# Kernel optimization log

Hardware: AMD Instinct MI355X
Metric: run time of the kernel (lower is better)

The kernel has to match this reference:

```python
import jax, jax.numpy as jnp
import numpy as np

N, E, IN, HID, HEADS, OUT = 50000, 800000, 184, 64, 4, 2
LRELU_SLOPE = 0.2
LN_EPS = 1e-5


def setup_inputs() -> dict:
    key = jax.random.key(0)
    ks = jax.random.split(key, 20)
    p = lambda k, s: jax.random.normal(k, s, jnp.float32) * 0.05
    return {
        'x': jax.random.normal(ks[0], (N, IN), jnp.float32),
        'edge_index': jax.random.randint(ks[1], (2, E), 0, N, jnp.int64),
        'Wp': p(ks[2], (IN, HID)), 'bp': p(ks[3], (HID,)),
        'W0': p(ks[4], (HID, HEADS * HID)), 'as0': p(ks[5], (HEADS, HID)), 'ad0': p(ks[6], (HEADS, HID)), 'b0': p(ks[7], (HEADS * HID,)),
        'W1': p(ks[8], (HEADS * HID, HEADS * HID)), 'as1': p(ks[9], (HEADS, HID)), 'ad1': p(ks[10], (HEADS, HID)), 'b1': p(ks[11], (HEADS * HID,)),
        'W2': p(ks[12], (HEADS * HID, OUT)), 'as2': p(ks[13], (1, OUT)), 'ad2': p(ks[14], (1, OUT)), 'b2': p(ks[15], (OUT,)),
        'ln_g': jnp.ones((HEADS * HID,), jnp.float32), 'ln_b': jnp.zeros((HEADS * HID,), jnp.float32),
    }


def _layernorm(x, g, b):
    mu = jnp.mean(x, axis=-1, keepdims=True)
    var = jnp.mean(jnp.square(x - mu), axis=-1, keepdims=True)
    return (x - mu) * jax.lax.rsqrt(var + LN_EPS) * g + b


def _gat_conv(x, src, dst, n, W, a_s, a_d, b, heads, c):
    # x: [n, in]; PyG GATConv: per-head linear, edge attention, segment softmax over dst, scatter-add
    h = (x @ W).reshape(n, heads, c)                 # [n, H, C]
    al_s = jnp.sum(h * a_s, axis=-1)                  # [n, H]
    al_d = jnp.sum(h * a_d, axis=-1)                  # [n, H]
    e = jax.nn.leaky_relu(al_s[src] + al_d[dst], LRELU_SLOPE)   # [E, H]
    m = jax.ops.segment_max(e, dst, num_segments=n)   # per-dst max (self-loops ensure nonempty)
    ex = jnp.exp(e - m[dst])
    den = jax.ops.segment_sum(ex, dst, num_segments=n)
    alpha = ex / (den[dst] + 1e-16)                   # PyG softmax eps
    msg = h[src] * alpha[:, :, None]                  # [E, H, C]
    out = jax.ops.segment_sum(msg, dst, num_segments=n)
    return out.reshape(n, heads * c) + b


def reference(x, edge_index, Wp, bp, W0, as0, ad0, b0, W1, as1, ad1, b1, W2, as2, ad2, b2, ln_g, ln_b):
    n = x.shape[0]
    loop = jnp.arange(n, dtype=edge_index.dtype)      # add_self_loops=True
    src = jnp.concatenate([edge_index[0], loop])
    dst = jnp.concatenate([edge_index[1], loop])

    h = x @ Wp + bp                                   # input_proj -> [n, HID]
    # layer 0: out dim HID*HEADS==256 -> norm; residual skipped (x_res is [n, HID])
    h = _gat_conv(h, src, dst, n, W0, as0, ad0, b0, HEADS, HID)
    h = jax.nn.elu(_layernorm(h, ln_g, ln_b))
    # dropout: eval mode (identity)
    # layer 1: norm + residual + elu
    h_res = h
    h = _gat_conv(h, src, dst, n, W1, as1, ad1, b1, HEADS, HID)
    h = jax.nn.elu(_layernorm(h, ln_g, ln_b) + h_res)
    # layer 2 (last): heads=1, no norm/activation
    return _gat_conv(h, src, dst, n, W2, as2, ad2, b2, 1, OUT)
```

## Files before the change

### kernel.cpp

```cpp
#include <hip/hip_runtime.h>
#include <hip/hip_bf16.h>
#include <cmath>
#include <cfloat>

constexpr int IN_DIM = 184;
constexpr int KP     = 192;
constexpr int HID    = 64;
constexpr int HEADS  = 4;
constexpr int F1     = HEADS * HID;
constexpr float SLOPE = 0.2f;
constexpr float LN_EPS = 1e-5f;

using short8 = __attribute__((ext_vector_type(8))) short;
using f32x4  = __attribute__((ext_vector_type(4))) float;

__device__ inline float b2f(ushort u) {
    return __uint_as_float(((unsigned)u) << 16);
}
__device__ inline ushort f2b(float f) {
    __hip_bfloat16 b = __float2bfloat16(f);
    return *reinterpret_cast<ushort*>(&b);
}
__device__ inline float lrelu(float e) { return e > 0.f ? e : SLOPE * e; }
__device__ inline float fexp(float x) { return __expf(x); }
__device__ inline float frcp(float x) { return __builtin_amdgcn_rcpf(x); }

__device__ inline size_t frag_idx(int k, int c) {
    int kt = k >> 5, kk = k & 31;
    int q = (kk & 15) >> 2, j = (kk & 3) | ((kk >> 4) << 2);
    int w = c >> 6, ct = (c >> 4) & 3, lr = c & 15;
    int lane = (q << 4) | lr;
    return ((((size_t)kt * 4 + w) * 4 + ct) * 64 + lane) * 8 + j;
}

__device__ inline void edge_sd(const int* __restrict__ ei, int E, int idx, int& s, int& d) {
    if (idx < E) { s = ei[idx]; d = ei[E + idx]; }
    else         { s = idx - E; d = idx - E; }
}

__global__ __launch_bounds__(256) void weight_prep(const float* __restrict__ Wp,
                                                   const float* __restrict__ W0,
                                                   const float* __restrict__ bp,
                                                   const float* __restrict__ W1,
                                                   ushort* __restrict__ Wf0,
                                                   float* __restrict__ bc,
                                                   ushort* __restrict__ Wf1,
                                                   const int* __restrict__ ei,
                                                   int E, int Etot,
                                                   int* __restrict__ deg) {
    int b = blockIdx.x, c = threadIdx.x;
    if (b < KP) {
        int k = b;
        float s = 0.f;
        if (k < IN_DIM)
            for (int j = 0; j < HID; ++j) s = fmaf(Wp[k * HID + j], W0[j * F1 + c], s);
        Wf0[frag_idx(k, c)] = f2b(s);
        if (k == 0) {
            float bs = 0.f;
            for (int j = 0; j < HID; ++j) bs = fmaf(bp[j], W0[j * F1 + c], bs);
            bc[c] = bs;
        }
    } else if (b < KP + F1) {
        int k = b - KP;
        Wf1[frag_idx(k, c)] = f2b(W1[(size_t)k * F1 + c]);
    } else {
        int idx = (b - KP - F1) * 256 + c;
        if (idx < Etot) {
            int s, d; edge_sd(ei, E, idx, s, d);
            atomicAdd(&deg[d], 1);
        }
    }
}

template<int KSTEPS, bool L0>
__global__ __launch_bounds__(256) void mfma_gemm2(const void* __restrict__ Xv,
                                                  const ushort* __restrict__ Wfrag,
                                                  const float* __restrict__ bc,
                                                  const float* __restrict__ as_,
                                                  const float* __restrict__ ad_,
                                                  unsigned char* __restrict__ F8,
                                                  float* __restrict__ rscale,
                                                  float* __restrict__ als,
                                                  float* __restrict__ ald,
                                                  int M,
                                                  int gemm_blocks,
                                                  const int* __restrict__ ei,
                                                  int E, int Etot,
                                                  int* __restrict__ wcur,
                                                  int* __restrict__ csr_src) {
    const int tid = threadIdx.x;
    int tile;

    if constexpr (L0) {
        const int bid = blockIdx.x;
        const int gq = bid / 3, gr = bid - gq * 3;
        const bool is_gemm = (gr == 0) && (gq < gemm_blocks);
        if (!is_gemm) {
            int fid = bid - min(gq + (gr ? 1 : 0) + (gr == 0 ? 1 : 0) - (gr == 0 ? 1 : 0), 0);
            int ng = min(gq + (gr > 0 ? 1 : 0), gemm_blocks);
            if (gr == 0 && gq >= gemm_blocks) ng = gemm_blocks;
            fid = bid - ng - (gr == 0 && gq < gemm_blocks ? 1 : 0);
            int base = fid * 512 + tid;
#pragma unroll
            for (int r = 0; r < 2; ++r) {
                int idx = base + r * 256;
                if (idx < Etot) {
                    int s, d; edge_sd(ei, E, idx, s, d);
                    int pos = atomicAdd(&wcur[d], 1);
                    csr_src[pos] = s;
                }
            }
            return;
        }
        tile = gq;
    } else {
        tile = blockIdx.x;
    }

    const int w = tid >> 6, l = tid & 63;
    const int lr = l & 15, q = l >> 4;
    const int row0 = tile * 64;

    __shared__ ushort a_lds[2][64][40];
    __shared__ float rmax_lds[64][4];

    const int srow = tid >> 2, seg = tid & 3;
    int grow = row0 + srow; if (grow >= M) grow = M - 1;

    auto stage = [&](int buf, int kt) {
        if constexpr (!L0) {
            const ushort* p = (const ushort*)Xv + (size_t)grow * 256 + kt * 32 + seg * 8;
            *(uint4*)&a_lds[buf][srow][seg * 8] = *(const uint4*)p;
        } else {
            int kb = kt * 32 + seg * 8;
            uint4 o = {0u, 0u, 0u, 0u};
            if (kb < IN_DIM) {
                const float* p = (const float*)Xv + (size_t)grow * IN_DIM + kb;
                float4 lo = *(const float4*)p;
                float4 hi = *(const float4*)(p + 4);
                o.x = (uint)f2b(lo.x) | ((uint)f2b(lo.y) << 16);
                o.y = (uint)f2b(lo.z) | ((uint)f2b(lo.w) << 16);
                o.z = (uint)f2b(hi.x) | ((uint)f2b(hi.y) << 16);
                o.w = (uint)f2b(hi.z) | ((uint)f2b(hi.w) << 16);
            }
            *(uint4*)&a_lds[buf][srow][seg * 8] = o;
        }
    };

    f32x4 acc[4][4] = {};

    stage(0, 0);
    short8 bcur[4];
#pragma unroll
    for (int ct = 0; ct < 4; ++ct) {
        const ushort* bp = Wfrag + ((((size_t)0 * 4 + w) * 4 + ct) * 64 + l) * 8;
        short8 b; *(uint4*)&b = *(const uint4*)bp; bcur[ct] = b;
    }
    __syncthreads();

    int buf = 0;
#pragma unroll
    for (int kt = 0; kt < KSTEPS; ++kt) {
        short8 bnext[4];
        if (kt + 1 < KSTEPS) {
#pragma unroll
            for (int ct = 0; ct < 4; ++ct) {
                const ushort* bp = Wfrag + ((((size_t)(kt + 1) * 4 + w) * 4 + ct) * 64 + l) * 8;
                short8 b; *(uint4*)&b = *(const uint4*)bp; bnext[ct] = b;
            }
            stage(buf ^ 1, kt + 1);
        }
        short8 afr[4];
#pragma unroll
        for (int rt = 0; rt < 4; ++rt) {
            short8 a;
            *(uint2*)&a       = *(const uint2*)&a_lds[buf][rt * 16 + lr][4 * q];
            *((uint2*)&a + 1) = *(const uint2*)&a_lds[buf][rt * 16 + lr][4 * q + 16];
            afr[rt] = a;
        }
#pragma unroll
        for (int rt = 0; rt < 4; ++rt)
#pragma unroll
            for (int ct = 0; ct < 4; ++ct)
                acc[rt][ct] = __builtin_amdgcn_mfma_f32_16x16x32_bf16(afr[rt], bcur[ct], acc[rt][ct], 0, 0, 0);
        __syncthreads();
        if (kt + 1 < KSTEPS) {
#pragma unroll
            for (int ct = 0; ct < 4; ++ct) bcur[ct] = bnext[ct];
        }
        buf ^= 1;
    }

    if constexpr (L0) {
        float bcv[4];
#pragma unroll
        for (int ct = 0; ct < 4; ++ct) bcv[ct] = bc[w * 64 + ct * 16 + lr];
#pragma unroll
        for (int rt = 0; rt < 4; ++rt)
#pragma unroll
            for (int ct = 0; ct < 4; ++ct)
#pragma unroll
                for (int r = 0; r < 4; ++r) acc[rt][ct][r] += bcv[ct];
    }

#pragma unroll
    for (int rt = 0; rt < 4; ++rt) {
#pragma unroll
        for (int r = 0; r < 4; ++r) {
            float m = fmaxf(fmaxf(fabsf(acc[rt][0][r]), fabsf(acc[rt][1][r])),
                            fmaxf(fabsf(acc[rt][2][r]), fabsf(acc[rt][3][r])));
            m = fmaxf(m, __shfl_xor(m, 1));
            m = fmaxf(m, __shfl_xor(m, 2));
            m = fmaxf(m, __shfl_xor(m, 4));
            m = fmaxf(m, __shfl_xor(m, 8));
            if (lr == 0) rmax_lds[rt * 16 + q * 4 + r][w] = m;
        }
    }
    __syncthreads();

#pragma unroll
    for (int rt = 0; rt < 4; ++rt) {
#pragma unroll
        for (int r = 0; r < 4; ++r) {
            int lrow = rt * 16 + q * 4 + r;
            float m = fmaxf(fmaxf(rmax_lds[lrow][0], rmax_lds[lrow][1]),
                            fmaxf(rmax_lds[lrow][2], rmax_lds[lrow][3]));
            float inv = (m > 0.f) ? 127.f / m : 0.f;
            int row = row0 + lrow;
            if (row < M) {
#pragma unroll
                for (int ct = 0; ct < 4; ++ct) {
                    int qv = (int)rintf(acc[rt][ct][r] * inv) + 128;
                    qv = min(max(qv, 0), 255);
                    F8[(size_t)row * 256 + w * 64 + ct * 16 + lr] = (unsigned char)qv;
                }
                if (w == 0 && lr == 0) rscale[row] = m * (1.f / 127.f);
            }
        }
    }

    float asv[4], adv[4];
#pragma unroll
    for (int ct = 0; ct < 4; ++ct) {
        asv[ct] = as_[w * 64 + ct * 16 + lr];
        adv[ct] = ad_[w * 64 + ct * 16 + lr];
    }
#pragma unroll
    for (int rt = 0; rt < 4; ++rt) {
#pragma unroll
        for (int r = 0; r < 4; ++r) {
            float ls = 0.f, ld_ = 0.f;
#pragma unroll
            for (int ct = 0; ct < 4; ++ct) {
                ls  = fmaf(acc[rt][ct][r], asv[ct], ls);
                ld_ = fmaf(acc[rt][ct][r], adv[ct], ld_);
            }
            for (int off = 8; off; off >>= 1) {
                ls  += __shfl_xor(ls, off);
                ld_ += __shfl_xor(ld_, off);
            }
            int row = row0 + rt * 16 + q * 4 + r;
            if (lr == 0 && row < M) {
                als[row * HEADS + w] = ls;
                ald[row * HEADS + w] = ld_;
            }
        }
    }
}

__global__ __launch_bounds__(256) void scan1(const int* __restrict__ deg, int* __restrict__ out,
                                             int* __restrict__ csum, int N) {
    __shared__ int s[256];
    int t = threadIdx.x;
    int idx0 = blockIdx.x * 1024 + t * 4;
    int v[4];
#pragma unroll
    for (int i = 0; i < 4; ++i) { int id = idx0 + i; v[i] = (id < N) ? deg[id] : 0; }
    int sum = v[0] + v[1] + v[2] + v[3];
    s[t] = sum; __syncthreads();
    for (int off = 1; off < 256; off <<= 1) {
        int x = (t >= off) ? s[t - off] : 0;
        __syncthreads();
        s[t] += x;
        __syncthreads();
    }
    int run = (t == 0) ? 0 : s[t - 1];
#pragma unroll
    for (int i = 0; i < 4; ++i) {
        run += v[i];
        int id = idx0 + i;
        if (id < N) out[id] = run;
    }
    if (t == 255) csum[blockIdx.x] = s[255];
}

__global__ __launch_bounds__(256) void scan3(const int* __restrict__ deg, int* __restrict__ rend,
                                             const int* __restrict__ csum, int* __restrict__ wcur, int N) {
    int id = blockIdx.x * 256 + threadIdx.x;
    if (id >= N) return;
    int chunk = id >> 10;
    int off = 0;
    for (int i = 0; i < chunk; ++i) off += csum[i];
    int e = rend[id] + off;
    rend[id] = e;
    wcur[id] = e - deg[id];
}

template<bool RES, bool FEAT2>
__global__ __launch_bounds__(128) void aggregate_fused(const int* __restrict__ csr_src,
                                                       const int* __restrict__ rend,
                                                       const int* __restrict__ deg_,
                                                       const unsigned char* __restrict__ feat,
                                                       const float* __restrict__ rscale,
                                                       const float* __restrict__ als,
                                                       const float* __restrict__ ald,
                                                       const float* __restrict__ bias,
                                                       const float* __restrict__ g,
                                                       const float* __restrict__ bln,
                                                       const ushort* __restrict__ res,
                                                       ushort* __restrict__ out_bf,
                                                       const float* __restrict__ W2,
                                                       const float* __restrict__ as2,
                                                       const float* __restrict__ ad2,
                                                       float4* __restrict__ nf2,
                                                       int N) {
    __shared__ __align__(16) float alds[2][64][4];
    __shared__ int srcs[2][64];
    const int w = threadIdx.x >> 6, l = threadIdx.x & 63;
    const int n = blockIdx.x * 2 + w;
    if (n >= N) return;
    const int dg = deg_[n], end = rend[n], start = end - dg;
    const int hf = l >> 5;
    const int lh = l & 31;
    const int hh = lh >> 3;
    const float4 ad4 = ((const float4*)ald)[n];

    float acc[8] = {0.f, 0.f, 0.f, 0.f, 0.f, 0.f, 0.f, 0.f};
    float accC = 0.f;

    auto fma8 = [&](uint2 u, float b) {
        acc[0] = fmaf((float)( u.x        & 0xffu), b, acc[0]);
        acc[1] = fmaf((float)((u.x >>  8) & 0xffu), b, acc[1]);
        acc[2] = fmaf((float)((u.x >> 16) & 0xffu), b, acc[2]);
        acc[3] = fmaf((float)( u.x >> 24         ), b, acc[3]);
        acc[4] = fmaf((float)( u.y        & 0xffu), b, acc[4]);
        acc[5] = fmaf((float)((u.y >>  8) & 0xffu), b, acc[5]);
        acc[6] = fmaf((float)((u.y >> 16) & 0xffu), b, acc[6]);
        acc[7] = fmaf((float)( u.y >> 24         ), b, acc[7]);
        accC += b;
    };

    auto LD = [&](int j) -> uint2 {
        int s = srcs[w][j];
        return *(const uint2*)&feat[(size_t)s * 256 + lh * 8];
    };

    auto gather_chunk = [&](int cnt) {
        int j = hf;
        for (; j + 2 < cnt; j += 4) {
            uint2 u0 = LD(j);
            uint2 u1 = LD(j + 2);
            fma8(u0, alds[w][j][hh]);
            fma8(u1, alds[w][j + 2][hh]);
        }
        for (; j < cnt; j += 2) {
            uint2 u0 = LD(j);
            fma8(u0, alds[w][j][hh]);
        }
    };

    if (dg <= 64) {
        int s = 0;
        float sc = 0.f;
        float4 ex = { 0.f, 0.f, 0.f, 0.f };
        if (l < dg) {
            s = csr_src[start + l];
            float4 a = ((const float4*)als)[s];
            sc = rscale[s];
            ex.x = fexp(lrelu(a.x + ad4.x));
            ex.y = fexp(lrelu(a.y + ad4.y));
            ex.z = fexp(lrelu(a.z + ad4.z));
            ex.w = fexp(lrelu(a.w + ad4.w));
        }
        float4 sum = ex;
        for (int off = 32; off; off >>= 1) {
            sum.x += __shfl_xor(sum.x, off);
            sum.y += __shfl_xor(sum.y, off);
            sum.z += __shfl_xor(sum.z, off);
            sum.w += __shfl_xor(sum.w, off);
        }
        float4 al = { ex.x * frcp(sum.x + 1e-16f) * sc, ex.y * frcp(sum.y + 1e-16f) * sc,
                      ex.z * frcp(sum.z + 1e-16f) * sc, ex.w * frcp(sum.w + 1e-16f) * sc };
        *(float4*)&alds[w][l][0] = al;
        srcs[w][l] = s;
        __builtin_amdgcn_s_waitcnt(0);
        gather_chunk(dg);
    } else {
        float4 sum = { 0.f, 0.f, 0.f, 0.f };
        for (int i = l; i < dg; i += 64) {
            int s = csr_src[start + i];
            float4 a = ((const float4*)als)[s];
            sum.x += fexp(lrelu(a.x + ad4.x));
            sum.y += fexp(lrelu(a.y + ad4.y));
            sum.z += fexp(lrelu(a.z + ad4.z));
            sum.w += fexp(lrelu(a.w + ad4.w));
        }
        for (int off = 32; off; off >>= 1) {
            sum.x += __shfl_xor(sum.x, off);
            sum.y += __shfl_xor(sum.y, off);
            sum.z += __shfl_xor(sum.z, off);
            sum.w += __shfl_xor(sum.w, off);
        }
        float4 inv = { frcp(sum.x + 1e-16f), frcp(sum.y + 1e-16f),
                       frcp(sum.z + 1e-16f), frcp(sum.w + 1e-16f) };
        for (int c0 = start; c0 < end; c0 += 64) {
            int cnt = min(64, end - c0);
            if (l < cnt) {
                int s = csr_src[c0 + l];
                float4 a = ((const float4*)als)[s];
                float sc = rscale[s];
                float4 al = { fexp(lrelu(a.x + ad4.x)) * inv.x * sc,
                              fexp(lrelu(a.y + ad4.y)) * inv.y * sc,
                              fexp(lrelu(a.z + ad4.z)) * inv.z * sc,
                              fexp(lrelu(a.w + ad4.w)) * inv.w * sc };
                *(float4*)&alds[w][l][0] = al;
                srcs[w][l] = s;
            }
            __builtin_amdgcn_s_waitcnt(0);
            gather_chunk(cnt);
        }
    }

#pragma unroll
    for (int r = 0; r < 8; ++r) acc[r] += __shfl_xor(acc[r], 32);
    accC += __shfl_xor(accC, 32);

    float4 bv0 = ((const float4*)bias)[lh * 2];
    float4 bv1 = ((const float4*)bias)[lh * 2 + 1];
    float c128 = 128.f * accC;
    float v[8] = { acc[0] - c128 + bv0.x, acc[1] - c128 + bv0.y,
                   acc[2] - c128 + bv0.z, acc[3] - c128 + bv0.w,
                   acc[4] - c128 + bv1.x, acc[5] - c128 + bv1.y,
                   acc[6] - c128 + bv1.z, acc[7] - c128 + bv1.w };
    float sm = v[0] + v[1] + v[2] + v[3] + v[4] + v[5] + v[6] + v[7];
    for (int off = 32; off; off >>= 1) sm += __shfl_xor(sm, off);
    float mu = sm * (1.f / (2 * F1));
    float dv = 0.f;
#pragma unroll
    for (int r = 0; r < 8; ++r) { float d = v[r] - mu; dv += d * d; }
    for (int off = 32; off; off >>= 1) dv += __shfl_xor(dv, off);
    float rstd = rsqrtf(dv * (1.f / (2 * F1)) + LN_EPS);
    float4 gv0 = ((const float4*)g)[lh * 2],   gv1 = ((const float4*)g)[lh * 2 + 1];
    float4 lb0 = ((const float4*)bln)[lh * 2], lb1 = ((const float4*)bln)[lh * 2 + 1];
    float y[8];
    y[0] = (v[0] - mu) * rstd * gv0.x + lb0.x;
    y[1] = (v[1] - mu) * rstd * gv0.y + lb0.y;
    y[2] = (v[2] - mu) * rstd * gv0.z + lb0.z;
    y[3] = (v[3] - mu) * rstd * gv0.w + lb0.w;
    y[4] = (v[4] - mu) * rstd * gv1.x + lb1.x;
    y[5] = (v[5] - mu) * rstd * gv1.y + lb1.y;
    y[6] = (v[6] - mu) * rstd * gv1.z + lb1.z;
    y[7] = (v[7] - mu) * rstd * gv1.w + lb1.w;
    if (RES) {
        uint4 rr = ((const uint4*)res)[(size_t)n * 32 + lh];
        y[0] += __uint_as_float(rr.x << 16);
        y[1] += __uint_as_float(rr.x & 0xffff0000u);
        y[2] += __uint_as_float(rr.y << 16);
        y[3] += __uint_as_float(rr.y & 0xffff0000u);
        y[4] += __uint_as_float(rr.z << 16);
        y[5] += __uint_as_float(rr.z & 0xffff0000u);
        y[6] += __uint_as_float(rr.w << 16);
        y[7] += __uint_as_float(rr.w & 0xffff0000u);
    }
#pragma unroll
    for (int r = 0; r < 8; ++r) y[r] = y[r] > 0.f ? y[r] : fexp(y[r]) - 1.f;

    if (!FEAT2) {
        if (l < 32) {
            uint4 o;
            o.x = (uint)f2b(y[0]) | ((uint)f2b(y[1]) << 16);
            o.y = (uint)f2b(y[2]) | ((uint)f2b(y[3]) << 16);
            o.z = (uint)f2b(y[4]) | ((uint)f2b(y[5]) << 16);
            o.w = (uint)f2b(y[6]) | ((uint)f2b(y[7]) << 16);
            ((uint4*)out_bf)[(size_t)n * 32 + lh] = o;
        }
    } else {
        const float4* W24 = (const float4*)W2;
        float c0 = 0.f, c1 = 0.f;
#pragma unroll
        for (int j = 0; j < 4; ++j) {
            float4 wv = W24[lh * 4 + j];
            c0 += y[2 * j] * wv.x + y[2 * j + 1] * wv.z;
            c1 += y[2 * j] * wv.y + y[2 * j + 1] * wv.w;
        }
        for (int off = 32; off; off >>= 1) {
            c0 += __shfl_xor(c0, off);
            c1 += __shfl_xor(c1, off);
        }
        c0 *= 0.5f; c1 *= 0.5f;
        if (l == 0) {
            float4 o = { c0, c1,
                         c0 * as2[0] + c1 * as2[1],
                         c0 * ad2[0] + c1 * ad2[1] };
            nf2[n] = o;
        }
    }
}

__global__ __launch_bounds__(128) void layer2_fused(const int* __restrict__ csr_src,
                                                    const int* __restrict__ rend,
                                                    const int* __restrict__ deg_,
                                                    const float4* __restrict__ nf2,
                                                    const float* __restrict__ b2,
                                                    float* __restrict__ out, int N) {
    const int w = threadIdx.x >> 6, l = threadIdx.x & 63;
    const int n = blockIdx.x * 2 + w;
    if (n >= N) return;
    const int dg = deg_[n], end = rend[n], start = end - dg;
    const float ad = nf2[n].w;

    float a0 = 0.f, a1 = 0.f;
    if (dg <= 64) {
        float ex = 0.f;
        float f0 = 0.f, f1 = 0.f;
        if (l < dg) {
            int s = csr_src[start + l];
            float4 v = nf2[s];
            ex = fexp(lrelu(v.z + ad));
            f0 = v.x; f1 = v.y;
        }
        float sum = ex;
        for (int off = 32; off; off >>= 1) sum += __shfl_xor(sum, off);
        float al = ex * frcp(sum + 1e-16f);
        a0 = f0 * al; a1 = f1 * al;
    } else {
        float sum = 0.f;
        for (int i = l; i < dg; i += 64) {
            int s = csr_src[start + i];
            sum += fexp(lrelu(nf2[s].z + ad));
        }
        for (int off = 32; off; off >>= 1) sum += __shfl_xor(sum, off);
        float inv = frcp(sum + 1e-16f);
        for (int i = l; i < dg; i += 64) {
            int s = csr_src[start + i];
            float4 v = nf2[s];
            float al = fexp(lrelu(v.z + ad)) * inv;
            a0 = fmaf(v.x, al, a0);
            a1 = fmaf(v.y, al, a1);
        }
    }
    for (int off = 32; off; off >>= 1) {
        a0 += __shfl_xor(a0, off);
        a1 += __shfl_xor(a1, off);
    }
    if (l == 0) {
        out[(size_t)n * 2 + 0] = a0 + b2[0];
        out[(size_t)n * 2 + 1] = a1 + b2[1];
    }
}

extern "C" void kernel_launch(void* const* d_in, const int* in_sizes, int n_in,
                              void* d_out, int out_size, void* d_ws, size_t ws_size,
                              hipStream_t stream) {
    const float* x    = (const float*)d_in[0];
    const int*   ei   = (const int*)d_in[1];
    const float* Wp   = (const float*)d_in[2];
    const float* bp   = (const float*)d_in[3];
    const float* W0   = (const float*)d_in[4];
    const float* as0  = (const float*)d_in[5];
    const float* ad0  = (const float*)d_in[6];
    const float* b0   = (const float*)d_in[7];
    const float* W1   = (const float*)d_in[8];
    const float* as1  = (const float*)d_in[9];
    const float* ad1  = (const float*)d_in[10];
    const float* b1   = (const float*)d_in[11];
    const float* W2   = (const float*)d_in[12];
    const float* as2  = (const float*)d_in[13];
    const float* ad2  = (const float*)d_in[14];
    const float* b2   = (const float*)d_in[15];
    const float* ln_g = (const float*)d_in[16];
    const float* ln_b = (const float*)d_in[17];
    float* out = (float*)d_out;

    const int N    = in_sizes[0] / IN_DIM;
    const int E    = in_sizes[1] / 2;
    const int Etot = E + N;

    char* wptr = (char*)d_ws;
    auto alloc = [&](size_t bytes) -> void* {
        void* p = wptr;
        wptr += (bytes + 255) & ~(size_t)255;
        return p;
    };
    unsigned char* F8 = (unsigned char*)alloc((size_t)N * F1);
    float*  rscale = (float*)alloc(sizeof(float) * (size_t)N);
    ushort* Ab     = (ushort*)alloc(sizeof(ushort) * (size_t)N * F1);
    float*  als    = (float*)alloc(sizeof(float) * (size_t)N * HEADS);
    float*  ald    = (float*)alloc(sizeof(float) * (size_t)N * HEADS);
    float4* nf2    = (float4*)alloc(sizeof(float4) * (size_t)N);
    ushort* Wf0    = (ushort*)alloc(sizeof(ushort) * (size_t)F1 * KP);
    float*  bc     = (float*)alloc(sizeof(float) * F1);
    ushort* Wf1    = (ushort*)alloc(sizeof(ushort) * (size_t)F1 * F1);
    int*    deg    = (int*)alloc(sizeof(int) * (size_t)N);
    int*    rend   = (int*)alloc(sizeof(int) * (size_t)N);
    int*    wcur   = (int*)alloc(sizeof(int) * (size_t)N);
    int*    csum   = (int*)alloc(sizeof(int) * 256);
    int*    csrs   = (int*)alloc(sizeof(int) * (size_t)Etot);

    const int eb   = (Etot + 255) / 256;
    const int eb2  = (Etot + 511) / 512;
    const int nb   = (N + 255) / 256;
    const int nb2  = (N + 1) / 2;
    const int nchunks = (N + 1023) / 1024;
    const int mb64 = (N + 63) / 64;

    hipMemsetAsync(deg, 0, sizeof(int) * (size_t)N, stream);
    weight_prep<<<KP + F1 + eb, 256, 0, stream>>>(Wp, W0, bp, W1, Wf0, bc, Wf1,
                                                  ei, E, Etot, deg);

    scan1<<<nchunks, 256, 0, stream>>>(deg, rend, csum, N);
    scan3<<<nb, 256, 0, stream>>>(deg, rend, csum, wcur, N);

    {
        int total = mb64 + eb2;
        mfma_gemm2<KP / 32, true><<<total, 256, 0, stream>>>(
            x, Wf0, bc, as0, ad0, F8, rscale, als, ald, N,
            mb64, ei, E, Etot, wcur, csrs);
    }
    aggregate_fused<false, false><<<nb2, 128, 0, stream>>>(csrs, rend, deg, F8, rscale,
        als, ald, b0, ln_g, ln_b, nullptr, Ab, nullptr, nullptr, nullptr, nullptr, N);

    mfma_gemm2<F1 / 32, false><<<mb64, 256, 0, stream>>>(
        Ab, Wf1, nullptr, as1, ad1, F8, rscale, als, ald, N,
        mb64, nullptr, 0, 0, nullptr, nullptr);
    aggregate_fused<true, true><<<nb2, 128, 0, stream>>>(csrs, rend, deg, F8, rscale,
        als, ald, b1, ln_g, ln_b, Ab, nullptr, W2, as2, ad2, nf2, N);

    layer2_fused<<<nb2, 128, 0, stream>>>(csrs, rend, deg, nf2, b2, out, N);
}
```

Before: 250.7 us.

## Pack bf16 source attention logits with row scale into one 16-byte record

New measurement: 258.2 us. 3.0% more time.

```diff
diff --git a/kernel.cpp b/kernel.cpp
--- a/kernel.cpp
+++ b/kernel.cpp
@@ -79,9 +79,8 @@
                                                   const float* __restrict__ as_,
                                                   const float* __restrict__ ad_,
                                                   unsigned char* __restrict__ F8,
-                                                  float* __restrict__ rscale,
-                                                  float* __restrict__ als,
-                                                  float* __restrict__ ald,
+                                                  uint4* __restrict__ pk,
+                                                  float4* __restrict__ ald4,
                                                   int M,
                                                   int gemm_blocks,
                                                   const int* __restrict__ ei,
@@ -93,23 +92,25 @@
 
     if constexpr (L0) {
         const int bid = blockIdx.x;
-        const int gq = bid / 3, gr = bid - gq * 3;
+        const int gq = bid >> 1, gr = bid & 1;
         const bool is_gemm = (gr == 0) && (gq < gemm_blocks);
         if (!is_gemm) {
-            int fid = bid - min(gq + (gr ? 1 : 0) + (gr == 0 ? 1 : 0) - (gr == 0 ? 1 : 0), 0);
-            int ng = min(gq + (gr > 0 ? 1 : 0), gemm_blocks);
-            if (gr == 0 && gq >= gemm_blocks) ng = gemm_blocks;
-            fid = bid - ng - (gr == 0 && gq < gemm_blocks ? 1 : 0);
-            int base = fid * 512 + tid;
-#pragma unroll
-            for (int r = 0; r < 2; ++r) {
+            int fid = bid - min((bid + 1) >> 1, gemm_blocks);
+            int base = fid * 1024 + tid;
+            int sv[4], pv[4];
+#pragma unroll
+            for (int r = 0; r < 4; ++r) {
                 int idx = base + r * 256;
+                sv[r] = -1;
                 if (idx < Etot) {
                     int s, d; edge_sd(ei, E, idx, s, d);
-                    int pos = atomicAdd(&wcur[d], 1);
-                    csr_src[pos] = s;
+                    sv[r] = s;
+                    pv[r] = atomicAdd(&wcur[d], 1);
                 }
             }
+#pragma unroll
+            for (int r = 0; r < 4; ++r)
+                if (sv[r] >= 0) csr_src[pv[r]] = sv[r];
             return;
         }
         tile = gq;
@@ -123,6 +124,8 @@
 
     __shared__ ushort a_lds[2][64][40];
     __shared__ float rmax_lds[64][4];
+    __shared__ float als_lds[64][4];
+    __shared__ float ald_lds[64][4];
 
     const int srow = tid >> 2, seg = tid & 3;
     int grow = row0 + srow; if (grow >= M) grow = M - 1;
@@ -234,7 +237,6 @@
                     qv = min(max(qv, 0), 255);
                     F8[(size_t)row * 256 + w * 64 + ct * 16 + lr] = (unsigned char)qv;
                 }
-                if (w == 0 && lr == 0) rscale[row] = m * (1.f / 127.f);
             }
         }
     }
@@ -259,11 +261,25 @@
                 ls  += __shfl_xor(ls, off);
                 ld_ += __shfl_xor(ld_, off);
             }
-            int row = row0 + rt * 16 + q * 4 + r;
-            if (lr == 0 && row < M) {
-                als[row * HEADS + w] = ls;
-                ald[row * HEADS + w] = ld_;
-            }
+            if (lr == 0) {
+                int lrow = rt * 16 + q * 4 + r;
+                als_lds[lrow][w] = ls;
+                ald_lds[lrow][w] = ld_;
+            }
+        }
+    }
+    __syncthreads();
+
+    if (tid < 64) {
+        int row = row0 + tid;
+        if (row < M) {
+            float m = fmaxf(fmaxf(rmax_lds[tid][0], rmax_lds[tid][1]),
+                            fmaxf(rmax_lds[tid][2], rmax_lds[tid][3]));
+            uint a01 = (uint)f2b(als_lds[tid][0]) | ((uint)f2b(als_lds[tid][1]) << 16);
+            uint a23 = (uint)f2b(als_lds[tid][2]) | ((uint)f2b(als_lds[tid][3]) << 16);
+            pk[row] = uint4{ a01, a23, __float_as_uint(m * (1.f / 127.f)), 0u };
+            ald4[row] = float4{ ald_lds[tid][0], ald_lds[tid][1],
+                                ald_lds[tid][2], ald_lds[tid][3] };
         }
     }
 }
@@ -311,9 +327,8 @@
                                                        const int* __restrict__ rend,
                                                        const int* __restrict__ deg_,
                                                        const unsigned char* __restrict__ feat,
-                                                       const float* __restrict__ rscale,
-                                                       const float* __restrict__ als,
-                                                       const float* __restrict__ ald,
+                                                       const uint4* __restrict__ pk,
+                                                       const float4* __restrict__ ald4,
                                                        const float* __restrict__ bias,
                                                        const float* __restrict__ g,
                                                        const float* __restrict__ bln,
@@ -333,7 +348,7 @@
     const int hf = l >> 5;
     const int lh = l & 31;
     const int hh = lh >> 3;
-    const float4 ad4 = ((const float4*)ald)[n];
+    const float4 ad4 = ald4[n];
 
     float acc[8] = {0.f, 0.f, 0.f, 0.f, 0.f, 0.f, 0.f, 0.f};
     float accC = 0.f;
@@ -369,18 +384,24 @@
         }
     };
 
+    auto exp4_of = [&](uint4 p) -> float4 {
+        float4 e;
+        e.x = fexp(lrelu(b2f((ushort)(p.x & 0xffff)) + ad4.x));
+        e.y = fexp(lrelu(b2f((ushort)(p.x >> 16))    + ad4.y));
+        e.z = fexp(lrelu(b2f((ushort)(p.y & 0xffff)) + ad4.z));
+        e.w = fexp(lrelu(b2f((ushort)(p.y >> 16))    + ad4.w));
+        return e;
+    };
+
     if (dg <= 64) {
         int s = 0;
         float sc = 0.f;
         float4 ex = { 0.f, 0.f, 0.f, 0.f };
         if (l < dg) {
             s = csr_src[start + l];
-            float4 a = ((const float4*)als)[s];
-            sc = rscale[s];
-            ex.x = fexp(lrelu(a.x + ad4.x));
-            ex.y = fexp(lrelu(a.y + ad4.y));
-            ex.z = fexp(lrelu(a.z + ad4.z));
-            ex.w = fexp(lrelu(a.w + ad4.w));
+            uint4 p = pk[s];
+            sc = __uint_as_float(p.z);
+            ex = exp4_of(p);
         }
         float4 sum = ex;
         for (int off = 32; off; off >>= 1) {
@@ -399,11 +420,8 @@
         float4 sum = { 0.f, 0.f, 0.f, 0.f };
         for (int i = l; i < dg; i += 64) {
             int s = csr_src[start + i];
-            float4 a = ((const float4*)als)[s];
-            sum.x += fexp(lrelu(a.x + ad4.x));
-            sum.y += fexp(lrelu(a.y + ad4.y));
-            sum.z += fexp(lrelu(a.z + ad4.z));
-            sum.w += fexp(lrelu(a.w + ad4.w));
+            float4 e = exp4_of(pk[s]);
+            sum.x += e.x; sum.y += e.y; sum.z += e.z; sum.w += e.w;
         }
         for (int off = 32; off; off >>= 1) {
             sum.x += __shfl_xor(sum.x, off);
@@ -417,12 +435,11 @@
             int cnt = min(64, end - c0);
             if (l < cnt) {
                 int s = csr_src[c0 + l];
-                float4 a = ((const float4*)als)[s];
-                float sc = rscale[s];
-                float4 al = { fexp(lrelu(a.x + ad4.x)) * inv.x * sc,
-                              fexp(lrelu(a.y + ad4.y)) * inv.y * sc,
-                              fexp(lrelu(a.z + ad4.z)) * inv.z * sc,
-                              fexp(lrelu(a.w + ad4.w)) * inv.w * sc };
+                uint4 p = pk[s];
+                float sc = __uint_as_float(p.z);
+                float4 e = exp4_of(p);
+                float4 al = { e.x * inv.x * sc, e.y * inv.y * sc,
+                              e.z * inv.z * sc, e.w * inv.w * sc };
                 *(float4*)&alds[w][l][0] = al;
                 srcs[w][l] = s;
             }
@@ -593,10 +610,9 @@
         return p;
     };
     unsigned char* F8 = (unsigned char*)alloc((size_t)N * F1);
-    float*  rscale = (float*)alloc(sizeof(float) * (size_t)N);
+    uint4*  pk     = (uint4*)alloc(sizeof(uint4) * (size_t)N);
+    float4* ald4   = (float4*)alloc(sizeof(float4) * (size_t)N);
     ushort* Ab     = (ushort*)alloc(sizeof(ushort) * (size_t)N * F1);
-    float*  als    = (float*)alloc(sizeof(float) * (size_t)N * HEADS);
-    float*  ald    = (float*)alloc(sizeof(float) * (size_t)N * HEADS);
     float4* nf2    = (float4*)alloc(sizeof(float4) * (size_t)N);
     ushort* Wf0    = (ushort*)alloc(sizeof(ushort) * (size_t)F1 * KP);
     float*  bc     = (float*)alloc(sizeof(float) * F1);
@@ -608,7 +624,7 @@
     int*    csrs   = (int*)alloc(sizeof(int) * (size_t)Etot);
 
     const int eb   = (Etot + 255) / 256;
-    const int eb2  = (Etot + 511) / 512;
+    const int eb4  = (Etot + 1023) / 1024;
     const int nb   = (N + 255) / 256;
     const int nb2  = (N + 1) / 2;
     const int nchunks = (N + 1023) / 1024;
@@ -621,20 +637,17 @@
     scan1<<<nchunks, 256, 0, stream>>>(deg, rend, csum, N);
     scan3<<<nb, 256, 0, stream>>>(deg, rend, csum, wcur, N);
 
-    {
-        int total = mb64 + eb2;
-        mfma_gemm2<KP / 32, true><<<total, 256, 0, stream>>>(
-            x, Wf0, bc, as0, ad0, F8, rscale, als, ald, N,
-            mb64, ei, E, Etot, wcur, csrs);
-    }
-    aggregate_fused<false, false><<<nb2, 128, 0, stream>>>(csrs, rend, deg, F8, rscale,
-        als, ald, b0, ln_g, ln_b, nullptr, Ab, nullptr, nullptr, nullptr, nullptr, N);
+    mfma_gemm2<KP / 32, true><<<mb64 + eb4, 256, 0, stream>>>(
+        x, Wf0, bc, as0, ad0, F8, pk, ald4, N,
+        mb64, ei, E, Etot, wcur, csrs);
+    aggregate_fused<false, false><<<nb2, 128, 0, stream>>>(csrs, rend, deg, F8, pk, ald4,
+        b0, ln_g, ln_b, nullptr, Ab, nullptr, nullptr, nullptr, nullptr, N);
 
     mfma_gemm2<F1 / 32, false><<<mb64, 256, 0, stream>>>(
-        Ab, Wf1, nullptr, as1, ad1, F8, rscale, als, ald, N,
+        Ab, Wf1, nullptr, as1, ad1, F8, pk, ald4, N,
         mb64, nullptr, 0, 0, nullptr, nullptr);
-    aggregate_fused<true, true><<<nb2, 128, 0, stream>>>(csrs, rend, deg, F8, rscale,
-        als, ald, b1, ln_g, ln_b, Ab, nullptr, W2, as2, ad2, nf2, N);
+    aggregate_fused<true, true><<<nb2, 128, 0, stream>>>(csrs, rend, deg, F8, pk, ald4,
+        b1, ln_g, ln_b, Ab, nullptr, W2, as2, ad2, nf2, N);
 
     layer2_fused<<<nb2, 128, 0, stream>>>(csrs, rend, deg, nf2, b2, out, N);
 }
```
